# Kernel optimization log

Hardware: AMD Instinct MI355X
Metric: run time of the kernel (lower is better)

## Reference

```python
import jax, jax.numpy as jnp
import numpy as np
import math

B, S, IN_DIM = 4, 2048, 256
ATT_DIM, NUM_HEADS, TOP_K = 128, 4, 32


def _linear_params(key, out_dim, in_dim):
    kw, kb = jax.random.split(key)
    bound = 1.0 / math.sqrt(in_dim)
    w = jax.random.uniform(kw, (out_dim, in_dim), jnp.float32, -bound, bound)
    b = jax.random.uniform(kb, (out_dim,), jnp.float32, -bound, bound)
    return w, b


def setup_inputs() -> dict:
    key = jax.random.key(0)
    keys = jax.random.split(key, 16)
    x = jax.random.normal(keys[0], (B, S, IN_DIM), jnp.float32)
    tp_w, tp_b = _linear_params(keys[1], ATT_DIM, IN_DIM)
    sp_w, sp_b = _linear_params(keys[2], ATT_DIM, IN_DIM)
    ta_qw, ta_qb = _linear_params(keys[3], ATT_DIM, ATT_DIM)
    ta_kw, ta_kb = _linear_params(keys[4], ATT_DIM, ATT_DIM)
    ta_vw, ta_vb = _linear_params(keys[5], ATT_DIM, ATT_DIM)
    ta_ow, ta_ob = _linear_params(keys[6], ATT_DIM, ATT_DIM)
    sa_qw, sa_qb = _linear_params(keys[7], ATT_DIM, ATT_DIM)
    sa_kw, sa_kb = _linear_params(keys[8], ATT_DIM, ATT_DIM)
    sa_vw, sa_vb = _linear_params(keys[9], ATT_DIM, ATT_DIM)
    sa_ow, sa_ob = _linear_params(keys[10], ATT_DIM, ATT_DIM)
    gate_w, gate_b = _linear_params(keys[11], ATT_DIM, 2 * ATT_DIM)
    fus_w, fus_b = _linear_params(keys[12], ATT_DIM, 2 * ATT_DIM)
    return dict(x=x, tp_w=tp_w, tp_b=tp_b, sp_w=sp_w, sp_b=sp_b,
                ta_qw=ta_qw, ta_qb=ta_qb, ta_kw=ta_kw, ta_kb=ta_kb,
                ta_vw=ta_vw, ta_vb=ta_vb, ta_ow=ta_ow, ta_ob=ta_ob,
                sa_qw=sa_qw, sa_qb=sa_qb, sa_kw=sa_kw, sa_kb=sa_kb,
                sa_vw=sa_vw, sa_vb=sa_vb, sa_ow=sa_ow, sa_ob=sa_ob,
                gate_w=gate_w, gate_b=gate_b, fus_w=fus_w, fus_b=fus_b)


def _lin(x, w, b):
    return x @ w.T + b


def _sparse_topk_attention(x, qw, qb, kw, kb, vw, vb, ow, ob):
    # x: [B, S, E]; dropout is identity in eval mode
    b, s, e = x.shape
    h, d = NUM_HEADS, e // NUM_HEADS
    q = _lin(x, qw, qb).reshape(b, s, h, d).transpose(0, 2, 1, 3)  # [B,H,S,D]
    k = _lin(x, kw, kb).reshape(b, s, h, d).transpose(0, 2, 1, 3)
    v = _lin(x, vw, vb).reshape(b, s, h, d).transpose(0, 2, 1, 3)
    scores = jnp.einsum('bhqd,bhkd->bhqk', q, k) / math.sqrt(d)  # [B,H,S,S]
    kk = min(TOP_K, s)
    top_scores, top_idx = jax.lax.top_k(scores, kk)  # [B,H,S,K]
    soft = jax.nn.softmax(top_scores, axis=-1)
    # scatter softmaxed top-k weights into a zero [B,H,S,S] matrix (faithful to source)
    bi = jnp.arange(b)[:, None, None, None]
    hi = jnp.arange(h)[None, :, None, None]
    si = jnp.arange(s)[None, None, :, None]
    sparse = jnp.zeros_like(scores).at[bi, hi, si, top_idx].set(soft)
    out = jnp.einsum('bhqk,bhkd->bhqd', sparse, v)
    out = out.transpose(0, 2, 1, 3).reshape(b, s, e)
    return _lin(out, ow, ob)


def reference(x, tp_w, tp_b, sp_w, sp_b,
              ta_qw, ta_qb, ta_kw, ta_kb, ta_vw, ta_vb, ta_ow, ta_ob,
              sa_qw, sa_qb, sa_kw, sa_kb, sa_vw, sa_vb, sa_ow, sa_ob,
              gate_w, gate_b, fus_w, fus_b):
    temporal = _lin(x, tp_w, tp_b)
    temporal = _sparse_topk_attention(temporal, ta_qw, ta_qb, ta_kw, ta_kb,
                                      ta_vw, ta_vb, ta_ow, ta_ob)
    semantic = _lin(x, sp_w, sp_b)
    semantic = _sparse_topk_attention(semantic, sa_qw, sa_qb, sa_kw, sa_kb,
                                      sa_vw, sa_vb, sa_ow, sa_ob)
    concat = jnp.concatenate([temporal, semantic], axis=-1)  # [B,S,2A]
    gate = jax.nn.sigmoid(_lin(concat, gate_w, gate_b))
    fused = _lin(concat, fus_w, fus_b) * gate
    return fused
```

## Files before the change

### kernel.cpp

```cpp
#include <hip/hip_runtime.h>
#include <math.h>

#define B_   4
#define S_   2048
#define AD   128
#define NH   4
#define HD   32
#define TK   32
#define SEG  1048576
#define CAP  192

#define OFF_PROJ 0
#define OFF_Q    (1 * SEG)
#define OFF_K    (2 * SEG)
#define OFF_V    (3 * SEG)
#define OFF_ATT  (4 * SEG)
#define OFF_T    (5 * SEG)
#define OFF_SB   (6 * SEG)
#define OFF_CAT  (7 * SEG)

__device__ float g_ws[9 * SEG];
__device__ float g_sc[8 * S_ * S_];

__device__ __forceinline__ unsigned f2key(float s) {
    unsigned u = __float_as_uint(s);
    return (u & 0x80000000u) ? ~u : (u | 0x80000000u);
}
__device__ __forceinline__ float key2f(unsigned k) {
    unsigned u = (k & 0x80000000u) ? (k & 0x7FFFFFFFu) : ~k;
    return __uint_as_float(u);
}

template <int KD>
__global__ __launch_bounds__(256)
void lin_kernel(const float* __restrict__ Xext, int xoff,
                const float* __restrict__ W, const float* __restrict__ Bv,
                int yoff)
{
    const float* X = Xext ? Xext : (const float*)(g_ws + xoff);
    float* Y = g_ws + yoff;
    __shared__ float Xs[32][68];
    __shared__ float Ws[32][68];
    const int bm = blockIdx.x * 64;
    const int bn = blockIdx.y * 64;
    const int t  = threadIdx.x;
    const int tx = t & 15, ty = t >> 4;
    const int sr = t >> 3, sc4 = t & 7;
    float acc[4][4] = {};
    for (int kk = 0; kk < KD; kk += 32) {
        #pragma unroll
        for (int it = 0; it < 2; ++it) {
            int rr = sr + it * 32;
            float4 xa = *(const float4*)(X + (size_t)(bm + rr) * KD + kk + sc4 * 4);
            float4 wa = *(const float4*)(W + (size_t)(bn + rr) * KD + kk + sc4 * 4);
            Xs[sc4*4+0][rr] = xa.x; Xs[sc4*4+1][rr] = xa.y;
            Xs[sc4*4+2][rr] = xa.z; Xs[sc4*4+3][rr] = xa.w;
            Ws[sc4*4+0][rr] = wa.x; Ws[sc4*4+1][rr] = wa.y;
            Ws[sc4*4+2][rr] = wa.z; Ws[sc4*4+3][rr] = wa.w;
        }
        __syncthreads();
        #pragma unroll
        for (int kc = 0; kc < 32; ++kc) {
            float4 a4 = *(const float4*)&Xs[kc][ty * 4];
            float4 b4 = *(const float4*)&Ws[kc][tx * 4];
            float a[4] = {a4.x, a4.y, a4.z, a4.w};
            float bb[4] = {b4.x, b4.y, b4.z, b4.w};
            #pragma unroll
            for (int i = 0; i < 4; ++i)
                #pragma unroll
                for (int j = 0; j < 4; ++j)
                    acc[i][j] = fmaf(a[i], bb[j], acc[i][j]);
        }
        __syncthreads();
    }
    #pragma unroll
    for (int i = 0; i < 4; ++i) {
        int row = bm + ty * 4 + i;
        int col = bn + tx * 4;
        float4 o;
        o.x = acc[i][0] + Bv[col + 0]; o.y = acc[i][1] + Bv[col + 1];
        o.z = acc[i][2] + Bv[col + 2]; o.w = acc[i][3] + Bv[col + 3];
        *(float4*)(Y + (size_t)row * AD + col) = o;
    }
}

template <int KD>
__global__ __launch_bounds__(256)
void lin3_kernel(int xoff,
                 const float* __restrict__ W0, const float* __restrict__ B0, int y0,
                 const float* __restrict__ W1, const float* __restrict__ B1, int y1,
                 const float* __restrict__ W2, const float* __restrict__ B2, int y2)
{
    const int z = blockIdx.z;
    const float* X = (const float*)(g_ws + xoff);
    const float* W = (z == 0) ? W0 : (z == 1) ? W1 : W2;
    const float* Bv = (z == 0) ? B0 : (z == 1) ? B1 : B2;
    float* Y = g_ws + ((z == 0) ? y0 : (z == 1) ? y1 : y2);
    __shared__ float Xs[32][68];
    __shared__ float Ws[32][68];
    const int bm = blockIdx.x * 64;
    const int bn = blockIdx.y * 64;
    const int t  = threadIdx.x;
    const int tx = t & 15, ty = t >> 4;
    const int sr = t >> 3, sc4 = t & 7;
    float acc[4][4] = {};
    for (int kk = 0; kk < KD; kk += 32) {
        #pragma unroll
        for (int it = 0; it < 2; ++it) {
            int rr = sr + it * 32;
            float4 xa = *(const float4*)(X + (size_t)(bm + rr) * KD + kk + sc4 * 4);
            float4 wa = *(const float4*)(W + (size_t)(bn + rr) * KD + kk + sc4 * 4);
            Xs[sc4*4+0][rr] = xa.x; Xs[sc4*4+1][rr] = xa.y;
            Xs[sc4*4+2][rr] = xa.z; Xs[sc4*4+3][rr] = xa.w;
            Ws[sc4*4+0][rr] = wa.x; Ws[sc4*4+1][rr] = wa.y;
            Ws[sc4*4+2][rr] = wa.z; Ws[sc4*4+3][rr] = wa.w;
        }
        __syncthreads();
        #pragma unroll
        for (int kc = 0; kc < 32; ++kc) {
            float4 a4 = *(const float4*)&Xs[kc][ty * 4];
            float4 b4 = *(const float4*)&Ws[kc][tx * 4];
            float a[4] = {a4.x, a4.y, a4.z, a4.w};
            float bb[4] = {b4.x, b4.y, b4.z, b4.w};
            #pragma unroll
            for (int i = 0; i < 4; ++i)
                #pragma unroll
                for (int j = 0; j < 4; ++j)
                    acc[i][j] = fmaf(a[i], bb[j], acc[i][j]);
        }
        __syncthreads();
    }
    #pragma unroll
    for (int i = 0; i < 4; ++i) {
        int row = bm + ty * 4 + i;
        int col = bn + tx * 4;
        float4 o;
        o.x = acc[i][0] + Bv[col + 0]; o.y = acc[i][1] + Bv[col + 1];
        o.z = acc[i][2] + Bv[col + 2]; o.w = acc[i][3] + Bv[col + 3];
        *(float4*)(Y + (size_t)row * AD + col) = o;
    }
}

__global__ __launch_bounds__(256)
void score_kernel(int qoff, int koff, int chunk)
{
    const int zh = blockIdx.z;
    const int hh = chunk * 8 + zh, b = hh >> 2, h = hh & 3;
    const float* Qb = g_ws + qoff + (size_t)b * S_ * AD + h * HD;
    const float* Kb = g_ws + koff + (size_t)b * S_ * AD + h * HD;
    float* Sc = g_sc + (size_t)zh * S_ * S_;
    __shared__ float Qs[32][68];
    __shared__ float Ks[32][68];
    const int t = threadIdx.x, tx = t & 15, ty = t >> 4;
    const int sr = t >> 3, sc4 = t & 7;
    const int q0 = blockIdx.y * 64, k0 = blockIdx.x * 64;
    #pragma unroll
    for (int it = 0; it < 2; ++it) {
        int rr = sr + it * 32;
        float4 qa = *(const float4*)(Qb + (size_t)(q0 + rr) * AD + sc4 * 4);
        float4 ka = *(const float4*)(Kb + (size_t)(k0 + rr) * AD + sc4 * 4);
        Qs[sc4*4+0][rr] = qa.x; Qs[sc4*4+1][rr] = qa.y;
        Qs[sc4*4+2][rr] = qa.z; Qs[sc4*4+3][rr] = qa.w;
        Ks[sc4*4+0][rr] = ka.x; Ks[sc4*4+1][rr] = ka.y;
        Ks[sc4*4+2][rr] = ka.z; Ks[sc4*4+3][rr] = ka.w;
    }
    __syncthreads();
    float acc[4][4] = {};
    #pragma unroll
    for (int kc = 0; kc < 32; ++kc) {
        float4 a4 = *(const float4*)&Qs[kc][ty * 4];
        float4 b4 = *(const float4*)&Ks[kc][tx * 4];
        float a[4] = {a4.x, a4.y, a4.z, a4.w};
        float bb[4] = {b4.x, b4.y, b4.z, b4.w};
        #pragma unroll
        for (int i = 0; i < 4; ++i)
            #pragma unroll
            for (int j = 0; j < 4; ++j)
                acc[i][j] = fmaf(a[i], bb[j], acc[i][j]);
    }
    const float scale = 0.17677669529663688f;
    #pragma unroll
    for (int i = 0; i < 4; ++i) {
        float4 o;
        o.x = acc[i][0] * scale; o.y = acc[i][1] * scale;
        o.z = acc[i][2] * scale; o.w = acc[i][3] * scale;
        *(float4*)(Sc + (size_t)(q0 + ty * 4 + i) * S_ + k0 + tx * 4) = o;
    }
}

__global__ __launch_bounds__(256)
void topk_kernel(int voff, int ooff, int chunk)
{
    const float* V = g_ws + voff;
    float* O = g_ws + ooff;

    __shared__ unsigned long long sve[4][CAP];
    __shared__ float    wsel[4][32];
    __shared__ unsigned jsel[4][32];

    const int wid  = threadIdx.x >> 6;
    const int lane = threadIdx.x & 63;
    const int gr   = blockIdx.x * 4 + wid;
    const int zh   = gr >> 11, q = gr & 2047;
    const int hh   = chunk * 8 + zh;
    const int b    = hh >> 2,  h = hh & 3;

    unsigned long long* sv = sve[wid];
    float*    wp = wsel[wid];
    unsigned* jp = jsel[wid];

    const float* Srow  = g_sc + (size_t)zh * S_ * S_ + (size_t)q * S_;
    const float* vbase = V + (size_t)b * S_ * AD + h * HD;

    float4 s4[8];
    #pragma unroll
    for (int i = 0; i < 8; ++i) s4[i] = ((const float4*)Srow)[i * 64 + lane];
    unsigned keys[32];
    unsigned lmax = 0u;
    #pragma unroll
    for (int i = 0; i < 8; ++i) {
        unsigned k0 = f2key(s4[i].x), k1 = f2key(s4[i].y);
        unsigned k2 = f2key(s4[i].z), k3 = f2key(s4[i].w);
        keys[i * 4 + 0] = k0; keys[i * 4 + 1] = k1;
        keys[i * 4 + 2] = k2; keys[i * 4 + 3] = k3;
        unsigned m01 = (k0 > k1) ? k0 : k1;
        unsigned m23 = (k2 > k3) ? k2 : k3;
        unsigned m = (m01 > m23) ? m01 : m23;
        lmax = (m > lmax) ? m : lmax;
    }

    unsigned bs = lmax;
    #pragma unroll
    for (int k = 2; k <= 64; k <<= 1) {
        #pragma unroll
        for (int j = k >> 1; j > 0; j >>= 1) {
            unsigned o = (unsigned)__shfl_xor((int)bs, j);
            bool up = ((lane & k) == 0);
            bool lower = ((lane & j) == 0);
            bs = (up == lower) ? (bs < o ? bs : o) : (bs > o ? bs : o);
        }
    }
    const unsigned thr  = (unsigned)__shfl((int)bs, 32);
    const unsigned mkey = (unsigned)__shfl((int)bs, 63);
    const float Mf = key2f(mkey);

    int base = 0;
    const unsigned long long lt = (1ull << lane) - 1ull;
    #pragma unroll
    for (int t = 0; t < 32; ++t) {
        bool pred = keys[t] >= thr;
        unsigned long long m = __ballot(pred);
        int slot = base + __popcll(m & lt);
        if (pred && slot < CAP) {
            unsigned jidx = (unsigned)((t >> 2) * 256 + lane * 4 + (t & 3));
            sv[slot] = ((unsigned long long)keys[t] << 32) | (unsigned)(2047 - jidx);
        }
        base += __popcll(m);
    }
    const int S = base;
    asm volatile("s_waitcnt lgkmcnt(0)" ::: "memory");

    if (S <= 64) {
        unsigned long long pi = (lane < S) ? sv[lane] : 0ull;
        int rank = 0;
        for (int jx = 0; jx < S; ++jx)
            rank += (sv[jx] > pi) ? 1 : 0;
        float e = 0.f; unsigned ji = 0;
        if (lane < S && rank < TK) {
            float val = key2f((unsigned)(pi >> 32));
            e = __expf(val - Mf);
            ji = 2047u - (unsigned)(pi & 0xFFFFFFFFull);
        }
        float esum = e;
        #pragma unroll
        for (int off = 1; off < 64; off <<= 1) esum += __shfl_xor(esum, off);
        if (lane < S && rank < TK) { wp[rank] = e / esum; jp[rank] = ji; }
    } else if (S <= CAP) {
        unsigned long long pi[3]; int rk[3]; float ee[3]; unsigned jj[3];
        float esum = 0.f;
        #pragma unroll
        for (int u = 0; u < 3; ++u) {
            int i = lane + u * 64;
            pi[u] = (i < S) ? sv[i] : 0ull;
            rk[u] = 0; ee[u] = 0.f; jj[u] = 0;
        }
        for (int jx = 0; jx < S; ++jx) {
            unsigned long long pj = sv[jx];
            #pragma unroll
            for (int u = 0; u < 3; ++u)
                rk[u] += (pj > pi[u]) ? 1 : 0;
        }
        #pragma unroll
        for (int u = 0; u < 3; ++u) {
            int i = lane + u * 64;
            if (i < S && rk[u] < TK) {
                float val = key2f((unsigned)(pi[u] >> 32));
                ee[u] = __expf(val - Mf);
                jj[u] = 2047u - (unsigned)(pi[u] & 0xFFFFFFFFull);
                esum += ee[u];
            }
        }
        #pragma unroll
        for (int off = 1; off < 64; off <<= 1) esum += __shfl_xor(esum, off);
        #pragma unroll
        for (int u = 0; u < 3; ++u) {
            int i = lane + u * 64;
            if (i < S && rk[u] < TK) { wp[rk[u]] = ee[u] / esum; jp[rk[u]] = jj[u]; }
        }
    } else {
        unsigned consumed = 0u;
        for (int i = 0; i < TK; ++i) {
            unsigned bk = 0u; unsigned gj = 0xFFFFFFFFu;
            #pragma unroll
            for (int t = 0; t < 32; ++t) {
                if (((consumed >> t) & 1u) == 0u) {
                    unsigned kk = keys[t];
                    unsigned j = (unsigned)((t >> 2) * 256 + lane * 4 + (t & 3));
                    if (kk > bk || (kk == bk && j < gj)) { bk = kk; gj = j; }
                }
            }
            #pragma unroll
            for (int off = 1; off < 64; off <<= 1) {
                unsigned ok = (unsigned)__shfl_xor((int)bk, off);
                unsigned oj = (unsigned)__shfl_xor((int)gj, off);
                if (ok > bk || (ok == bk && oj < gj)) { bk = ok; gj = oj; }
            }
            if (((gj >> 2) & 63u) == (unsigned)lane && gj != 0xFFFFFFFFu) {
                int t = ((int)gj >> 8) * 4 + ((int)gj & 3);
                consumed |= (1u << t);
            }
            if (lane == 0) { wp[i] = key2f(bk); jp[i] = gj; }
        }
        asm volatile("s_waitcnt lgkmcnt(0)" ::: "memory");
        float v = (lane < TK) ? wp[lane] : 0.f;
        float e = (lane < TK) ? __expf(v - Mf) : 0.f;
        float esum = e;
        #pragma unroll
        for (int off = 1; off < 64; off <<= 1) esum += __shfl_xor(esum, off);
        if (lane < TK) wp[lane] = e / esum;
    }
    asm volatile("s_waitcnt lgkmcnt(0)" ::: "memory");

    float oacc = 0.f;
    const int dd = lane & 31, half = lane >> 5;
    #pragma unroll
    for (int u2 = 0; u2 < 16; ++u2) {
        int i = half * 16 + u2;
        oacc = fmaf(wp[i], vbase[(size_t)jp[i] * AD + dd], oacc);
    }
    oacc += __shfl_down(oacc, 32);
    if (lane < HD) O[((size_t)b * S_ + q) * AD + h * HD + lane] = oacc;
}

__global__ __launch_bounds__(256)
void concat_kernel()
{
    int i = blockIdx.x * 256 + threadIdx.x;
    int row = i >> 8, c = i & 255;
    float v = (c < AD) ? g_ws[OFF_T + row * AD + c]
                       : g_ws[OFF_SB + row * AD + (c - AD)];
    g_ws[OFF_CAT + i] = v;
}

__global__ __launch_bounds__(256)
void fuse_kernel(float* __restrict__ out)
{
    int i = blockIdx.x * 256 + threadIdx.x;
    float g = g_ws[OFF_Q + i];
    float f = g_ws[OFF_K + i];
    out[i] = f / (1.0f + expf(-g));
}

extern "C" void kernel_launch(void* const* d_in, const int* in_sizes, int n_in,
                              void* d_out, int out_size, void* d_ws, size_t ws_size,
                              hipStream_t stream)
{
    (void)in_sizes; (void)n_in; (void)d_ws; (void)ws_size; (void)out_size;
    const float* x      = (const float*)d_in[0];
    const float* tp_w   = (const float*)d_in[1];
    const float* tp_b   = (const float*)d_in[2];
    const float* sp_w   = (const float*)d_in[3];
    const float* sp_b   = (const float*)d_in[4];
    const float* gate_w = (const float*)d_in[21];
    const float* gate_b = (const float*)d_in[22];
    const float* fus_w  = (const float*)d_in[23];
    const float* fus_b  = (const float*)d_in[24];

    dim3 gl(128, 2);
    for (int br = 0; br < 2; ++br) {
        const float* pw = br ? sp_w : tp_w;
        const float* pb = br ? sp_b : tp_b;
        int base = 5 + br * 8;
        const float* qw = (const float*)d_in[base + 0];
        const float* qb = (const float*)d_in[base + 1];
        const float* kw = (const float*)d_in[base + 2];
        const float* kb = (const float*)d_in[base + 3];
        const float* vw = (const float*)d_in[base + 4];
        const float* vb = (const float*)d_in[base + 5];
        const float* ow = (const float*)d_in[base + 6];
        const float* ob = (const float*)d_in[base + 7];

        lin_kernel<256><<<gl, 256, 0, stream>>>(x, 0, pw, pb, OFF_PROJ);
        lin3_kernel<128><<<dim3(128, 2, 3), 256, 0, stream>>>(
            OFF_PROJ, qw, qb, OFF_Q, kw, kb, OFF_K, vw, vb, OFF_V);
        for (int chunk = 0; chunk < 2; ++chunk) {
            score_kernel<<<dim3(32, 32, 8), 256, 0, stream>>>(OFF_Q, OFF_K, chunk);
            topk_kernel<<<4096, 256, 0, stream>>>(OFF_V, OFF_ATT, chunk);
        }
        lin_kernel<128><<<gl, 256, 0, stream>>>(nullptr, OFF_ATT, ow, ob,
                                                br ? OFF_SB : OFF_T);
    }
    concat_kernel<<<8192, 256, 0, stream>>>();
    lin3_kernel<256><<<dim3(128, 2, 2), 256, 0, stream>>>(
        OFF_CAT, gate_w, gate_b, OFF_Q, fus_w, fus_b, OFF_K,
        (const float*)nullptr, (const float*)nullptr, 0);
    fuse_kernel<<<4096, 256, 0, stream>>>((float*)d_out);
}
```

Before: 373.3 us.

## Process two score rows per wavefront in top-k and pad shared tiles

The top-k kernel now handles two query rows per wavefront. Both rows' keys are loaded and their bitonic threshold searches run interleaved, then selection runs per row, and each half-wave does the V gather for one row, which removes the cross-half shuffle reduction. This is meant to add instruction-level parallelism and halve the grid. The cost is doubled register use for keys (64 per lane), which may lower occupancy. Separately, the shared-memory tile padding changes from 68 to 72 floats in the GEMM and score kernels to alter the bank-conflict pattern.

```diff
diff --git a/kernel.cpp b/kernel.cpp
--- a/kernel.cpp
+++ b/kernel.cpp
@@ -39,8 +39,8 @@
 {
     const float* X = Xext ? Xext : (const float*)(g_ws + xoff);
     float* Y = g_ws + yoff;
-    __shared__ float Xs[32][68];
-    __shared__ float Ws[32][68];
+    __shared__ float Xs[32][72];
+    __shared__ float Ws[32][72];
     const int bm = blockIdx.x * 64;
     const int bn = blockIdx.y * 64;
     const int t  = threadIdx.x;
@@ -96,8 +96,8 @@
     const float* W = (z == 0) ? W0 : (z == 1) ? W1 : W2;
     const float* Bv = (z == 0) ? B0 : (z == 1) ? B1 : B2;
     float* Y = g_ws + ((z == 0) ? y0 : (z == 1) ? y1 : y2);
-    __shared__ float Xs[32][68];
-    __shared__ float Ws[32][68];
+    __shared__ float Xs[32][72];
+    __shared__ float Ws[32][72];
     const int bm = blockIdx.x * 64;
     const int bn = blockIdx.y * 64;
     const int t  = threadIdx.x;
@@ -149,8 +149,8 @@
     const float* Qb = g_ws + qoff + (size_t)b * S_ * AD + h * HD;
     const float* Kb = g_ws + koff + (size_t)b * S_ * AD + h * HD;
     float* Sc = g_sc + (size_t)zh * S_ * S_;
-    __shared__ float Qs[32][68];
-    __shared__ float Ks[32][68];
+    __shared__ float Qs[32][72];
+    __shared__ float Ks[32][72];
     const int t = threadIdx.x, tx = t & 15, ty = t >> 4;
     const int sr = t >> 3, sc4 = t & 7;
     const int q0 = blockIdx.y * 64, k0 = blockIdx.x * 64;
@@ -188,62 +188,11 @@
     }
 }
 
-__global__ __launch_bounds__(256)
-void topk_kernel(int voff, int ooff, int chunk)
-{
-    const float* V = g_ws + voff;
-    float* O = g_ws + ooff;
-
-    __shared__ unsigned long long sve[4][CAP];
-    __shared__ float    wsel[4][32];
-    __shared__ unsigned jsel[4][32];
-
-    const int wid  = threadIdx.x >> 6;
-    const int lane = threadIdx.x & 63;
-    const int gr   = blockIdx.x * 4 + wid;
-    const int zh   = gr >> 11, q = gr & 2047;
-    const int hh   = chunk * 8 + zh;
-    const int b    = hh >> 2,  h = hh & 3;
-
-    unsigned long long* sv = sve[wid];
-    float*    wp = wsel[wid];
-    unsigned* jp = jsel[wid];
-
-    const float* Srow  = g_sc + (size_t)zh * S_ * S_ + (size_t)q * S_;
-    const float* vbase = V + (size_t)b * S_ * AD + h * HD;
-
-    float4 s4[8];
-    #pragma unroll
-    for (int i = 0; i < 8; ++i) s4[i] = ((const float4*)Srow)[i * 64 + lane];
-    unsigned keys[32];
-    unsigned lmax = 0u;
-    #pragma unroll
-    for (int i = 0; i < 8; ++i) {
-        unsigned k0 = f2key(s4[i].x), k1 = f2key(s4[i].y);
-        unsigned k2 = f2key(s4[i].z), k3 = f2key(s4[i].w);
-        keys[i * 4 + 0] = k0; keys[i * 4 + 1] = k1;
-        keys[i * 4 + 2] = k2; keys[i * 4 + 3] = k3;
-        unsigned m01 = (k0 > k1) ? k0 : k1;
-        unsigned m23 = (k2 > k3) ? k2 : k3;
-        unsigned m = (m01 > m23) ? m01 : m23;
-        lmax = (m > lmax) ? m : lmax;
-    }
-
-    unsigned bs = lmax;
-    #pragma unroll
-    for (int k = 2; k <= 64; k <<= 1) {
-        #pragma unroll
-        for (int j = k >> 1; j > 0; j >>= 1) {
-            unsigned o = (unsigned)__shfl_xor((int)bs, j);
-            bool up = ((lane & k) == 0);
-            bool lower = ((lane & j) == 0);
-            bs = (up == lower) ? (bs < o ? bs : o) : (bs > o ? bs : o);
-        }
-    }
-    const unsigned thr  = (unsigned)__shfl((int)bs, 32);
-    const unsigned mkey = (unsigned)__shfl((int)bs, 63);
-    const float Mf = key2f(mkey);
-
+__device__ __forceinline__ void select_row(const unsigned (&keys)[32],
+                                           unsigned long long* sv,
+                                           float* wp, unsigned* jp,
+                                           int lane, unsigned thr, float Mf)
+{
     int base = 0;
     const unsigned long long lt = (1ull << lane) - 1ull;
     #pragma unroll
@@ -340,16 +289,83 @@
         if (lane < TK) wp[lane] = e / esum;
     }
     asm volatile("s_waitcnt lgkmcnt(0)" ::: "memory");
-
+}
+
+__global__ __launch_bounds__(256)
+void topk_kernel(int voff, int ooff, int chunk)
+{
+    const float* V = g_ws + voff;
+    float* O = g_ws + ooff;
+
+    __shared__ unsigned long long sve[4][2][CAP];
+    __shared__ float    wsel[4][2][32];
+    __shared__ unsigned jsel[4][2][32];
+
+    const int wid  = threadIdx.x >> 6;
+    const int lane = threadIdx.x & 63;
+    const int gr   = blockIdx.x * 4 + wid;
+    const int row0 = gr * 2;
+    const int zh   = row0 >> 11;
+    const int q0   = row0 & 2047, q1 = q0 + 1;
+    const int hh   = chunk * 8 + zh;
+    const int b    = hh >> 2,  h = hh & 3;
+
+    const float* Srow0 = g_sc + (size_t)zh * S_ * S_ + (size_t)q0 * S_;
+    const float* Srow1 = Srow0 + S_;
+    const float* vbase = V + (size_t)b * S_ * AD + h * HD;
+
+    unsigned keys0[32], keys1[32];
+    unsigned lmax0 = 0u, lmax1 = 0u;
+    #pragma unroll
+    for (int i = 0; i < 8; ++i) {
+        float4 s4 = ((const float4*)Srow0)[i * 64 + lane];
+        unsigned k0 = f2key(s4.x), k1 = f2key(s4.y);
+        unsigned k2 = f2key(s4.z), k3 = f2key(s4.w);
+        keys0[i*4+0] = k0; keys0[i*4+1] = k1; keys0[i*4+2] = k2; keys0[i*4+3] = k3;
+        unsigned m01 = (k0 > k1) ? k0 : k1, m23 = (k2 > k3) ? k2 : k3;
+        unsigned m = (m01 > m23) ? m01 : m23;
+        lmax0 = (m > lmax0) ? m : lmax0;
+    }
+    #pragma unroll
+    for (int i = 0; i < 8; ++i) {
+        float4 s4 = ((const float4*)Srow1)[i * 64 + lane];
+        unsigned k0 = f2key(s4.x), k1 = f2key(s4.y);
+        unsigned k2 = f2key(s4.z), k3 = f2key(s4.w);
+        keys1[i*4+0] = k0; keys1[i*4+1] = k1; keys1[i*4+2] = k2; keys1[i*4+3] = k3;
+        unsigned m01 = (k0 > k1) ? k0 : k1, m23 = (k2 > k3) ? k2 : k3;
+        unsigned m = (m01 > m23) ? m01 : m23;
+        lmax1 = (m > lmax1) ? m : lmax1;
+    }
+
+    unsigned bs0 = lmax0, bs1 = lmax1;
+    #pragma unroll
+    for (int k = 2; k <= 64; k <<= 1) {
+        #pragma unroll
+        for (int j = k >> 1; j > 0; j >>= 1) {
+            unsigned o0 = (unsigned)__shfl_xor((int)bs0, j);
+            unsigned o1 = (unsigned)__shfl_xor((int)bs1, j);
+            bool keepmin = (((lane & k) == 0) == ((lane & j) == 0));
+            bs0 = keepmin ? (bs0 < o0 ? bs0 : o0) : (bs0 > o0 ? bs0 : o0);
+            bs1 = keepmin ? (bs1 < o1 ? bs1 : o1) : (bs1 > o1 ? bs1 : o1);
+        }
+    }
+    const unsigned thr0 = (unsigned)__shfl((int)bs0, 32);
+    const unsigned thr1 = (unsigned)__shfl((int)bs1, 32);
+    const float Mf0 = key2f((unsigned)__shfl((int)bs0, 63));
+    const float Mf1 = key2f((unsigned)__shfl((int)bs1, 63));
+
+    select_row(keys0, sve[wid][0], wsel[wid][0], jsel[wid][0], lane, thr0, Mf0);
+    select_row(keys1, sve[wid][1], wsel[wid][1], jsel[wid][1], lane, thr1, Mf1);
+
+    const int dd = lane & 31, half = lane >> 5;
+    const float*    wp = wsel[wid][half];
+    const unsigned* jp = jsel[wid][half];
     float oacc = 0.f;
-    const int dd = lane & 31, half = lane >> 5;
-    #pragma unroll
-    for (int u2 = 0; u2 < 16; ++u2) {
-        int i = half * 16 + u2;
+    #pragma unroll
+    for (int i = 0; i < 32; ++i)
         oacc = fmaf(wp[i], vbase[(size_t)jp[i] * AD + dd], oacc);
-    }
-    oacc += __shfl_down(oacc, 32);
-    if (lane < HD) O[((size_t)b * S_ + q) * AD + h * HD + lane] = oacc;
+    const int qq = half ? q1 : q0;
+    O[((size_t)b * S_ + qq) * AD + h * HD + dd] = oacc;
 }
 
 __global__ __launch_bounds__(256)
@@ -405,7 +421,7 @@
             OFF_PROJ, qw, qb, OFF_Q, kw, kb, OFF_K, vw, vb, OFF_V);
         for (int chunk = 0; chunk < 2; ++chunk) {
             score_kernel<<<dim3(32, 32, 8), 256, 0, stream>>>(OFF_Q, OFF_K, chunk);
-            topk_kernel<<<4096, 256, 0, stream>>>(OFF_V, OFF_ATT, chunk);
+            topk_kernel<<<2048, 256, 0, stream>>>(OFF_V, OFF_ATT, chunk);
         }
         lin_kernel<128><<<gl, 256, 0, stream>>>(nullptr, OFF_ATT, ow, ob,
                                                 br ? OFF_SB : OFF_T);
```

New measurement: 429.0 us. 14.9% more time.

## Swizzle shared-memory tiles and halve score-buffer chunk size

Applied to the files above, without the earlier changes.

Applies an XOR swizzle to the transposed shared-memory tiles in the linear and score GEMM kernels to reduce LDS bank conflicts. It also cuts the per-launch head chunk from 8 to 4, shrinking the global score scratch buffer so it is more likely to stay cache-resident between the score and top-k passes. The cost is twice as many score/top-k launches, with smaller grids per launch.

```diff
diff --git a/kernel.cpp b/kernel.cpp
--- a/kernel.cpp
+++ b/kernel.cpp
@@ -9,6 +9,7 @@
 #define TK   32
 #define SEG  1048576
 #define CAP  192
+#define CHD  4
 
 #define OFF_PROJ 0
 #define OFF_Q    (1 * SEG)
@@ -20,7 +21,7 @@
 #define OFF_CAT  (7 * SEG)
 
 __device__ float g_ws[9 * SEG];
-__device__ float g_sc[8 * S_ * S_];
+__device__ float g_sc[CHD * S_ * S_];
 
 __device__ __forceinline__ unsigned f2key(float s) {
     unsigned u = __float_as_uint(s);
@@ -46,23 +47,26 @@
     const int t  = threadIdx.x;
     const int tx = t & 15, ty = t >> 4;
     const int sr = t >> 3, sc4 = t & 7;
+    const int ssw = sc4 << 2;
     float acc[4][4] = {};
     for (int kk = 0; kk < KD; kk += 32) {
         #pragma unroll
         for (int it = 0; it < 2; ++it) {
             int rr = sr + it * 32;
+            int rs = rr ^ ssw;
             float4 xa = *(const float4*)(X + (size_t)(bm + rr) * KD + kk + sc4 * 4);
             float4 wa = *(const float4*)(W + (size_t)(bn + rr) * KD + kk + sc4 * 4);
-            Xs[sc4*4+0][rr] = xa.x; Xs[sc4*4+1][rr] = xa.y;
-            Xs[sc4*4+2][rr] = xa.z; Xs[sc4*4+3][rr] = xa.w;
-            Ws[sc4*4+0][rr] = wa.x; Ws[sc4*4+1][rr] = wa.y;
-            Ws[sc4*4+2][rr] = wa.z; Ws[sc4*4+3][rr] = wa.w;
+            Xs[sc4*4+0][rs] = xa.x; Xs[sc4*4+1][rs] = xa.y;
+            Xs[sc4*4+2][rs] = xa.z; Xs[sc4*4+3][rs] = xa.w;
+            Ws[sc4*4+0][rs] = wa.x; Ws[sc4*4+1][rs] = wa.y;
+            Ws[sc4*4+2][rs] = wa.z; Ws[sc4*4+3][rs] = wa.w;
         }
         __syncthreads();
         #pragma unroll
         for (int kc = 0; kc < 32; ++kc) {
-            float4 a4 = *(const float4*)&Xs[kc][ty * 4];
-            float4 b4 = *(const float4*)&Ws[kc][tx * 4];
+            const int swz = ((kc >> 2) & 7) << 2;
+            float4 a4 = *(const float4*)&Xs[kc][(ty * 4) ^ swz];
+            float4 b4 = *(const float4*)&Ws[kc][(tx * 4) ^ swz];
             float a[4] = {a4.x, a4.y, a4.z, a4.w};
             float bb[4] = {b4.x, b4.y, b4.z, b4.w};
             #pragma unroll
@@ -103,23 +107,26 @@
     const int t  = threadIdx.x;
     const int tx = t & 15, ty = t >> 4;
     const int sr = t >> 3, sc4 = t & 7;
+    const int ssw = sc4 << 2;
     float acc[4][4] = {};
     for (int kk = 0; kk < KD; kk += 32) {
         #pragma unroll
         for (int it = 0; it < 2; ++it) {
             int rr = sr + it * 32;
+            int rs = rr ^ ssw;
             float4 xa = *(const float4*)(X + (size_t)(bm + rr) * KD + kk + sc4 * 4);
             float4 wa = *(const float4*)(W + (size_t)(bn + rr) * KD + kk + sc4 * 4);
-            Xs[sc4*4+0][rr] = xa.x; Xs[sc4*4+1][rr] = xa.y;
-            Xs[sc4*4+2][rr] = xa.z; Xs[sc4*4+3][rr] = xa.w;
-            Ws[sc4*4+0][rr] = wa.x; Ws[sc4*4+1][rr] = wa.y;
-            Ws[sc4*4+2][rr] = wa.z; Ws[sc4*4+3][rr] = wa.w;
+            Xs[sc4*4+0][rs] = xa.x; Xs[sc4*4+1][rs] = xa.y;
+            Xs[sc4*4+2][rs] = xa.z; Xs[sc4*4+3][rs] = xa.w;
+            Ws[sc4*4+0][rs] = wa.x; Ws[sc4*4+1][rs] = wa.y;
+            Ws[sc4*4+2][rs] = wa.z; Ws[sc4*4+3][rs] = wa.w;
         }
         __syncthreads();
         #pragma unroll
         for (int kc = 0; kc < 32; ++kc) {
-            float4 a4 = *(const float4*)&Xs[kc][ty * 4];
-            float4 b4 = *(const float4*)&Ws[kc][tx * 4];
+            const int swz = ((kc >> 2) & 7) << 2;
+            float4 a4 = *(const float4*)&Xs[kc][(ty * 4) ^ swz];
+            float4 b4 = *(const float4*)&Ws[kc][(tx * 4) ^ swz];
             float a[4] = {a4.x, a4.y, a4.z, a4.w};
             float bb[4] = {b4.x, b4.y, b4.z, b4.w};
             #pragma unroll
@@ -145,7 +152,7 @@
 void score_kernel(int qoff, int koff, int chunk)
 {
     const int zh = blockIdx.z;
-    const int hh = chunk * 8 + zh, b = hh >> 2, h = hh & 3;
+    const int hh = chunk * CHD + zh, b = hh >> 2, h = hh & 3;
     const float* Qb = g_ws + qoff + (size_t)b * S_ * AD + h * HD;
     const float* Kb = g_ws + koff + (size_t)b * S_ * AD + h * HD;
     float* Sc = g_sc + (size_t)zh * S_ * S_;
@@ -153,23 +160,26 @@
     __shared__ float Ks[32][68];
     const int t = threadIdx.x, tx = t & 15, ty = t >> 4;
     const int sr = t >> 3, sc4 = t & 7;
+    const int ssw = sc4 << 2;
     const int q0 = blockIdx.y * 64, k0 = blockIdx.x * 64;
     #pragma unroll
     for (int it = 0; it < 2; ++it) {
         int rr = sr + it * 32;
+        int rs = rr ^ ssw;
         float4 qa = *(const float4*)(Qb + (size_t)(q0 + rr) * AD + sc4 * 4);
         float4 ka = *(const float4*)(Kb + (size_t)(k0 + rr) * AD + sc4 * 4);
-        Qs[sc4*4+0][rr] = qa.x; Qs[sc4*4+1][rr] = qa.y;
-        Qs[sc4*4+2][rr] = qa.z; Qs[sc4*4+3][rr] = qa.w;
-        Ks[sc4*4+0][rr] = ka.x; Ks[sc4*4+1][rr] = ka.y;
-        Ks[sc4*4+2][rr] = ka.z; Ks[sc4*4+3][rr] = ka.w;
+        Qs[sc4*4+0][rs] = qa.x; Qs[sc4*4+1][rs] = qa.y;
+        Qs[sc4*4+2][rs] = qa.z; Qs[sc4*4+3][rs] = qa.w;
+        Ks[sc4*4+0][rs] = ka.x; Ks[sc4*4+1][rs] = ka.y;
+        Ks[sc4*4+2][rs] = ka.z; Ks[sc4*4+3][rs] = ka.w;
     }
     __syncthreads();
     float acc[4][4] = {};
     #pragma unroll
     for (int kc = 0; kc < 32; ++kc) {
-        float4 a4 = *(const float4*)&Qs[kc][ty * 4];
-        float4 b4 = *(const float4*)&Ks[kc][tx * 4];
+        const int swz = ((kc >> 2) & 7) << 2;
+        float4 a4 = *(const float4*)&Qs[kc][(ty * 4) ^ swz];
+        float4 b4 = *(const float4*)&Ks[kc][(tx * 4) ^ swz];
         float a[4] = {a4.x, a4.y, a4.z, a4.w};
         float bb[4] = {b4.x, b4.y, b4.z, b4.w};
         #pragma unroll
@@ -202,7 +212,7 @@
     const int lane = threadIdx.x & 63;
     const int gr   = blockIdx.x * 4 + wid;
     const int zh   = gr >> 11, q = gr & 2047;
-    const int hh   = chunk * 8 + zh;
+    const int hh   = chunk * CHD + zh;
     const int b    = hh >> 2,  h = hh & 3;
 
     unsigned long long* sv = sve[wid];
@@ -403,9 +413,9 @@
         lin_kernel<256><<<gl, 256, 0, stream>>>(x, 0, pw, pb, OFF_PROJ);
         lin3_kernel<128><<<dim3(128, 2, 3), 256, 0, stream>>>(
             OFF_PROJ, qw, qb, OFF_Q, kw, kb, OFF_K, vw, vb, OFF_V);
-        for (int chunk = 0; chunk < 2; ++chunk) {
-            score_kernel<<<dim3(32, 32, 8), 256, 0, stream>>>(OFF_Q, OFF_K, chunk);
-            topk_kernel<<<4096, 256, 0, stream>>>(OFF_V, OFF_ATT, chunk);
+        for (int chunk = 0; chunk < 4; ++chunk) {
+            score_kernel<<<dim3(32, 32, CHD), 256, 0, stream>>>(OFF_Q, OFF_K, chunk);
+            topk_kernel<<<CHD * 512, 256, 0, stream>>>(OFF_V, OFF_ATT, chunk);
         }
         lin_kernel<128><<<gl, 256, 0, stream>>>(nullptr, OFF_ATT, ow, ob,
                                                 br ? OFF_SB : OFF_T);
```

Result: slower. 442.8 us (+18.6%).

## Software-pipeline score and top-k stages in one interleaved kernel

Applied to the files above, without the earlier changes.

Merges the score GEMM and top-k/softmax/gather kernels into one pipe_kernel whose blocks are split between computing scores for the next chunk and running top-k on the previous chunk. Double-buffered score storage lets the two stages run concurrently, so compute-bound score tiles overlap with memory- and latency-bound top-k work. Both branches' Q/K/V projections are computed up front into separate buffers so chunks from the two attention branches can be chained. The cost is more workspace memory, shared memory sized to the larger role, and some divergence in the per-block role choice.

```diff
diff --git a/kernel.cpp b/kernel.cpp
--- a/kernel.cpp
+++ b/kernel.cpp
@@ -11,16 +11,20 @@
 #define CAP  192
 
 #define OFF_PROJ 0
-#define OFF_Q    (1 * SEG)
-#define OFF_K    (2 * SEG)
-#define OFF_V    (3 * SEG)
-#define OFF_ATT  (4 * SEG)
-#define OFF_T    (5 * SEG)
-#define OFF_SB   (6 * SEG)
-#define OFF_CAT  (7 * SEG)
-
-__device__ float g_ws[9 * SEG];
-__device__ float g_sc[8 * S_ * S_];
+#define OFF_QT  (1 * SEG)
+#define OFF_KT  (2 * SEG)
+#define OFF_VT  (3 * SEG)
+#define OFF_QS  (4 * SEG)
+#define OFF_KS  (5 * SEG)
+#define OFF_VS  (6 * SEG)
+#define OFF_AT  (7 * SEG)
+#define OFF_AS  (8 * SEG)
+#define OFF_T   (9 * SEG)
+#define OFF_SB  (10 * SEG)
+#define OFF_CAT (11 * SEG)
+
+__device__ float g_ws[13 * SEG];
+__device__ float g_sc[2][8 * S_ * S_];
 
 __device__ __forceinline__ unsigned f2key(float s) {
     unsigned u = __float_as_uint(s);
@@ -142,214 +146,223 @@
 }
 
 __global__ __launch_bounds__(256)
-void score_kernel(int qoff, int koff, int chunk)
-{
-    const int zh = blockIdx.z;
-    const int hh = chunk * 8 + zh, b = hh >> 2, h = hh & 3;
-    const float* Qb = g_ws + qoff + (size_t)b * S_ * AD + h * HD;
-    const float* Kb = g_ws + koff + (size_t)b * S_ * AD + h * HD;
-    float* Sc = g_sc + (size_t)zh * S_ * S_;
-    __shared__ float Qs[32][68];
-    __shared__ float Ks[32][68];
-    const int t = threadIdx.x, tx = t & 15, ty = t >> 4;
-    const int sr = t >> 3, sc4 = t & 7;
-    const int q0 = blockIdx.y * 64, k0 = blockIdx.x * 64;
-    #pragma unroll
-    for (int it = 0; it < 2; ++it) {
-        int rr = sr + it * 32;
-        float4 qa = *(const float4*)(Qb + (size_t)(q0 + rr) * AD + sc4 * 4);
-        float4 ka = *(const float4*)(Kb + (size_t)(k0 + rr) * AD + sc4 * 4);
-        Qs[sc4*4+0][rr] = qa.x; Qs[sc4*4+1][rr] = qa.y;
-        Qs[sc4*4+2][rr] = qa.z; Qs[sc4*4+3][rr] = qa.w;
-        Ks[sc4*4+0][rr] = ka.x; Ks[sc4*4+1][rr] = ka.y;
-        Ks[sc4*4+2][rr] = ka.z; Ks[sc4*4+3][rr] = ka.w;
+void pipe_kernel(int nscore, int ntopk,
+                 int s_qoff, int s_koff, int s_chunk, int s_buf,
+                 int t_voff, int t_ooff, int t_chunk, int t_buf)
+{
+    __shared__ __align__(16) unsigned char smem[17408];
+    const int bid = blockIdx.x;
+    bool isScore;
+    int rid;
+    if (nscore > 0 && ntopk > 0) {
+        if ((bid % 3) == 2) { isScore = false; rid = bid / 3; }
+        else                { isScore = true;  rid = (bid / 3) * 2 + (bid % 3); }
+    } else if (nscore > 0) { isScore = true;  rid = bid; }
+    else                   { isScore = false; rid = bid; }
+
+    if (isScore) {
+        float (*Qs)[68] = (float(*)[68])smem;
+        float (*Ks)[68] = (float(*)[68])(smem + 8704);
+        const int kx = rid & 31, qy = (rid >> 5) & 31, zh = rid >> 10;
+        const int hh = s_chunk * 8 + zh, b = hh >> 2, h = hh & 3;
+        const float* Qb = g_ws + s_qoff + (size_t)b * S_ * AD + h * HD;
+        const float* Kb = g_ws + s_koff + (size_t)b * S_ * AD + h * HD;
+        float* Sc = g_sc[s_buf] + (size_t)zh * S_ * S_;
+        const int t = threadIdx.x, tx = t & 15, ty = t >> 4;
+        const int sr = t >> 3, sc4 = t & 7;
+        const int q0 = qy * 64, k0 = kx * 64;
+        #pragma unroll
+        for (int it = 0; it < 2; ++it) {
+            int rr = sr + it * 32;
+            float4 qa = *(const float4*)(Qb + (size_t)(q0 + rr) * AD + sc4 * 4);
+            float4 ka = *(const float4*)(Kb + (size_t)(k0 + rr) * AD + sc4 * 4);
+            Qs[sc4*4+0][rr] = qa.x; Qs[sc4*4+1][rr] = qa.y;
+            Qs[sc4*4+2][rr] = qa.z; Qs[sc4*4+3][rr] = qa.w;
+            Ks[sc4*4+0][rr] = ka.x; Ks[sc4*4+1][rr] = ka.y;
+            Ks[sc4*4+2][rr] = ka.z; Ks[sc4*4+3][rr] = ka.w;
+        }
+        __syncthreads();
+        float acc[4][4] = {};
+        #pragma unroll
+        for (int kc = 0; kc < 32; ++kc) {
+            float4 a4 = *(const float4*)&Qs[kc][ty * 4];
+            float4 b4 = *(const float4*)&Ks[kc][tx * 4];
+            float a[4] = {a4.x, a4.y, a4.z, a4.w};
+            float bb[4] = {b4.x, b4.y, b4.z, b4.w};
+            #pragma unroll
+            for (int i = 0; i < 4; ++i)
+                #pragma unroll
+                for (int j = 0; j < 4; ++j)
+                    acc[i][j] = fmaf(a[i], bb[j], acc[i][j]);
+        }
+        const float scale = 0.17677669529663688f;
+        #pragma unroll
+        for (int i = 0; i < 4; ++i) {
+            float4 o;
+            o.x = acc[i][0] * scale; o.y = acc[i][1] * scale;
+            o.z = acc[i][2] * scale; o.w = acc[i][3] * scale;
+            *(float4*)(Sc + (size_t)(q0 + ty * 4 + i) * S_ + k0 + tx * 4) = o;
+        }
+    } else {
+        unsigned long long* sve = (unsigned long long*)smem;
+        float*    wsel = (float*)(smem + 6144);
+        unsigned* jsel = (unsigned*)(smem + 6656);
+        const float* V = g_ws + t_voff;
+        float* O = g_ws + t_ooff;
+
+        const int wid  = threadIdx.x >> 6;
+        const int lane = threadIdx.x & 63;
+        const int gr   = rid * 4 + wid;
+        const int zh   = gr >> 11, q = gr & 2047;
+        const int hh   = t_chunk * 8 + zh;
+        const int b    = hh >> 2,  h = hh & 3;
+
+        unsigned long long* sv = sve + wid * CAP;
+        float*    wp = wsel + wid * 32;
+        unsigned* jp = jsel + wid * 32;
+
+        const float* Srow  = g_sc[t_buf] + (size_t)zh * S_ * S_ + (size_t)q * S_;
+        const float* vbase = V + (size_t)b * S_ * AD + h * HD;
+
+        float4 s4[8];
+        #pragma unroll
+        for (int i = 0; i < 8; ++i) s4[i] = ((const float4*)Srow)[i * 64 + lane];
+        unsigned keys[32];
+        unsigned lmax = 0u;
+        #pragma unroll
+        for (int i = 0; i < 8; ++i) {
+            unsigned k0 = f2key(s4[i].x), k1 = f2key(s4[i].y);
+            unsigned k2 = f2key(s4[i].z), k3 = f2key(s4[i].w);
+            keys[i * 4 + 0] = k0; keys[i * 4 + 1] = k1;
+            keys[i * 4 + 2] = k2; keys[i * 4 + 3] = k3;
+            unsigned m01 = (k0 > k1) ? k0 : k1;
+            unsigned m23 = (k2 > k3) ? k2 : k3;
+            unsigned m = (m01 > m23) ? m01 : m23;
+            lmax = (m > lmax) ? m : lmax;
+        }
+
+        unsigned bs = lmax;
+        #pragma unroll
+        for (int k = 2; k <= 64; k <<= 1) {
+            #pragma unroll
+            for (int j = k >> 1; j > 0; j >>= 1) {
+                unsigned o = (unsigned)__shfl_xor((int)bs, j);
+                bool up = ((lane & k) == 0);
+                bool lower = ((lane & j) == 0);
+                bs = (up == lower) ? (bs < o ? bs : o) : (bs > o ? bs : o);
+            }
+        }
+        const unsigned thr  = (unsigned)__shfl((int)bs, 32);
+        const unsigned mkey = (unsigned)__shfl((int)bs, 63);
+        const float Mf = key2f(mkey);
+
+        int base = 0;
+        const unsigned long long lt = (1ull << lane) - 1ull;
+        #pragma unroll
+        for (int t = 0; t < 32; ++t) {
+            bool pred = keys[t] >= thr;
+            unsigned long long m = __ballot(pred);
+            int slot = base + __popcll(m & lt);
+            if (pred && slot < CAP) {
+                unsigned jidx = (unsigned)((t >> 2) * 256 + lane * 4 + (t & 3));
+                sv[slot] = ((unsigned long long)keys[t] << 32) | (unsigned)(2047 - jidx);
+            }
+            base += __popcll(m);
+        }
+        const int S = base;
+        asm volatile("s_waitcnt lgkmcnt(0)" ::: "memory");
+
+        if (S <= 64) {
+            unsigned long long pi = (lane < S) ? sv[lane] : 0ull;
+            int rank = 0;
+            for (int jx = 0; jx < S; ++jx)
+                rank += (sv[jx] > pi) ? 1 : 0;
+            float e = 0.f; unsigned ji = 0;
+            if (lane < S && rank < TK) {
+                float val = key2f((unsigned)(pi >> 32));
+                e = __expf(val - Mf);
+                ji = 2047u - (unsigned)(pi & 0xFFFFFFFFull);
+            }
+            float esum = e;
+            #pragma unroll
+            for (int off = 1; off < 64; off <<= 1) esum += __shfl_xor(esum, off);
+            if (lane < S && rank < TK) { wp[rank] = e / esum; jp[rank] = ji; }
+        } else if (S <= CAP) {
+            unsigned long long pi[3]; int rk[3]; float ee[3]; unsigned jj[3];
+            float esum = 0.f;
+            #pragma unroll
+            for (int u = 0; u < 3; ++u) {
+                int i = lane + u * 64;
+                pi[u] = (i < S) ? sv[i] : 0ull;
+                rk[u] = 0; ee[u] = 0.f; jj[u] = 0;
+            }
+            for (int jx = 0; jx < S; ++jx) {
+                unsigned long long pj = sv[jx];
+                #pragma unroll
+                for (int u = 0; u < 3; ++u)
+                    rk[u] += (pj > pi[u]) ? 1 : 0;
+            }
+            #pragma unroll
+            for (int u = 0; u < 3; ++u) {
+                int i = lane + u * 64;
+                if (i < S && rk[u] < TK) {
+                    float val = key2f((unsigned)(pi[u] >> 32));
+                    ee[u] = __expf(val - Mf);
+                    jj[u] = 2047u - (unsigned)(pi[u] & 0xFFFFFFFFull);
+                    esum += ee[u];
+                }
+            }
+            #pragma unroll
+            for (int off = 1; off < 64; off <<= 1) esum += __shfl_xor(esum, off);
+            #pragma unroll
+            for (int u = 0; u < 3; ++u) {
+                int i = lane + u * 64;
+                if (i < S && rk[u] < TK) { wp[rk[u]] = ee[u] / esum; jp[rk[u]] = jj[u]; }
+            }
+        } else {
+            unsigned consumed = 0u;
+            for (int i = 0; i < TK; ++i) {
+                unsigned bk = 0u; unsigned gj = 0xFFFFFFFFu;
+                #pragma unroll
+                for (int t = 0; t < 32; ++t) {
+                    if (((consumed >> t) & 1u) == 0u) {
+                        unsigned kk = keys[t];
+                        unsigned j = (unsigned)((t >> 2) * 256 + lane * 4 + (t & 3));
+                        if (kk > bk || (kk == bk && j < gj)) { bk = kk; gj = j; }
+                    }
+                }
+                #pragma unroll
+                for (int off = 1; off < 64; off <<= 1) {
+                    unsigned ok = (unsigned)__shfl_xor((int)bk, off);
+                    unsigned oj = (unsigned)__shfl_xor((int)gj, off);
+                    if (ok > bk || (ok == bk && oj < gj)) { bk = ok; gj = oj; }
+                }
+                if (((gj >> 2) & 63u) == (unsigned)lane && gj != 0xFFFFFFFFu) {
+                    int t = ((int)gj >> 8) * 4 + ((int)gj & 3);
+                    consumed |= (1u << t);
+                }
+                if (lane == 0) { wp[i] = key2f(bk); jp[i] = gj; }
+            }
+            asm volatile("s_waitcnt lgkmcnt(0)" ::: "memory");
+            float v = (lane < TK) ? wp[lane] : 0.f;
+            float e = (lane < TK) ? __expf(v - Mf) : 0.f;
+            float esum = e;
+            #pragma unroll
+            for (int off = 1; off < 64; off <<= 1) esum += __shfl_xor(esum, off);
+            if (lane < TK) wp[lane] = e / esum;
+        }
+        asm volatile("s_waitcnt lgkmcnt(0)" ::: "memory");
+
+        float oacc = 0.f;
+        const int dd = lane & 31, half = lane >> 5;
+        #pragma unroll
+        for (int u2 = 0; u2 < 16; ++u2) {
+            int i = half * 16 + u2;
+            oacc = fmaf(wp[i], vbase[(size_t)jp[i] * AD + dd], oacc);
+        }
+        oacc += __shfl_down(oacc, 32);
+        if (lane < HD) O[((size_t)b * S_ + q) * AD + h * HD + lane] = oacc;
     }
-    __syncthreads();
-    float acc[4][4] = {};
-    #pragma unroll
-    for (int kc = 0; kc < 32; ++kc) {
-        float4 a4 = *(const float4*)&Qs[kc][ty * 4];
-        float4 b4 = *(const float4*)&Ks[kc][tx * 4];
-        float a[4] = {a4.x, a4.y, a4.z, a4.w};
-        float bb[4] = {b4.x, b4.y, b4.z, b4.w};
-        #pragma unroll
-        for (int i = 0; i < 4; ++i)
-            #pragma unroll
-            for (int j = 0; j < 4; ++j)
-                acc[i][j] = fmaf(a[i], bb[j], acc[i][j]);
-    }
-    const float scale = 0.17677669529663688f;
-    #pragma unroll
-    for (int i = 0; i < 4; ++i) {
-        float4 o;
-        o.x = acc[i][0] * scale; o.y = acc[i][1] * scale;
-        o.z = acc[i][2] * scale; o.w = acc[i][3] * scale;
-        *(float4*)(Sc + (size_t)(q0 + ty * 4 + i) * S_ + k0 + tx * 4) = o;
-    }
-}
-
-__global__ __launch_bounds__(256)
-void topk_kernel(int voff, int ooff, int chunk)
-{
-    const float* V = g_ws + voff;
-    float* O = g_ws + ooff;
-
-    __shared__ unsigned long long sve[4][CAP];
-    __shared__ float    wsel[4][32];
-    __shared__ unsigned jsel[4][32];
-
-    const int wid  = threadIdx.x >> 6;
-    const int lane = threadIdx.x & 63;
-    const int gr   = blockIdx.x * 4 + wid;
-    const int zh   = gr >> 11, q = gr & 2047;
-    const int hh   = chunk * 8 + zh;
-    const int b    = hh >> 2,  h = hh & 3;
-
-    unsigned long long* sv = sve[wid];
-    float*    wp = wsel[wid];
-    unsigned* jp = jsel[wid];
-
-    const float* Srow  = g_sc + (size_t)zh * S_ * S_ + (size_t)q * S_;
-    const float* vbase = V + (size_t)b * S_ * AD + h * HD;
-
-    float4 s4[8];
-    #pragma unroll
-    for (int i = 0; i < 8; ++i) s4[i] = ((const float4*)Srow)[i * 64 + lane];
-    unsigned keys[32];
-    unsigned lmax = 0u;
-    #pragma unroll
-    for (int i = 0; i < 8; ++i) {
-        unsigned k0 = f2key(s4[i].x), k1 = f2key(s4[i].y);
-        unsigned k2 = f2key(s4[i].z), k3 = f2key(s4[i].w);
-        keys[i * 4 + 0] = k0; keys[i * 4 + 1] = k1;
-        keys[i * 4 + 2] = k2; keys[i * 4 + 3] = k3;
-        unsigned m01 = (k0 > k1) ? k0 : k1;
-        unsigned m23 = (k2 > k3) ? k2 : k3;
-        unsigned m = (m01 > m23) ? m01 : m23;
-        lmax = (m > lmax) ? m : lmax;
-    }
-
-    unsigned bs = lmax;
-    #pragma unroll
-    for (int k = 2; k <= 64; k <<= 1) {
-        #pragma unroll
-        for (int j = k >> 1; j > 0; j >>= 1) {
-            unsigned o = (unsigned)__shfl_xor((int)bs, j);
-            bool up = ((lane & k) == 0);
-            bool lower = ((lane & j) == 0);
-            bs = (up == lower) ? (bs < o ? bs : o) : (bs > o ? bs : o);
-        }
-    }
-    const unsigned thr  = (unsigned)__shfl((int)bs, 32);
-    const unsigned mkey = (unsigned)__shfl((int)bs, 63);
-    const float Mf = key2f(mkey);
-
-    int base = 0;
-    const unsigned long long lt = (1ull << lane) - 1ull;
-    #pragma unroll
-    for (int t = 0; t < 32; ++t) {
-        bool pred = keys[t] >= thr;
-        unsigned long long m = __ballot(pred);
-        int slot = base + __popcll(m & lt);
-        if (pred && slot < CAP) {
-            unsigned jidx = (unsigned)((t >> 2) * 256 + lane * 4 + (t & 3));
-            sv[slot] = ((unsigned long long)keys[t] << 32) | (unsigned)(2047 - jidx);
-        }
-        base += __popcll(m);
-    }
-    const int S = base;
-    asm volatile("s_waitcnt lgkmcnt(0)" ::: "memory");
-
-    if (S <= 64) {
-        unsigned long long pi = (lane < S) ? sv[lane] : 0ull;
-        int rank = 0;
-        for (int jx = 0; jx < S; ++jx)
-            rank += (sv[jx] > pi) ? 1 : 0;
-        float e = 0.f; unsigned ji = 0;
-        if (lane < S && rank < TK) {
-            float val = key2f((unsigned)(pi >> 32));
-            e = __expf(val - Mf);
-            ji = 2047u - (unsigned)(pi & 0xFFFFFFFFull);
-        }
-        float esum = e;
-        #pragma unroll
-        for (int off = 1; off < 64; off <<= 1) esum += __shfl_xor(esum, off);
-        if (lane < S && rank < TK) { wp[rank] = e / esum; jp[rank] = ji; }
-    } else if (S <= CAP) {
-        unsigned long long pi[3]; int rk[3]; float ee[3]; unsigned jj[3];
-        float esum = 0.f;
-        #pragma unroll
-        for (int u = 0; u < 3; ++u) {
-            int i = lane + u * 64;
-            pi[u] = (i < S) ? sv[i] : 0ull;
-            rk[u] = 0; ee[u] = 0.f; jj[u] = 0;
-        }
-        for (int jx = 0; jx < S; ++jx) {
-            unsigned long long pj = sv[jx];
-            #pragma unroll
-            for (int u = 0; u < 3; ++u)
-                rk[u] += (pj > pi[u]) ? 1 : 0;
-        }
-        #pragma unroll
-        for (int u = 0; u < 3; ++u) {
-            int i = lane + u * 64;
-            if (i < S && rk[u] < TK) {
-                float val = key2f((unsigned)(pi[u] >> 32));
-                ee[u] = __expf(val - Mf);
-                jj[u] = 2047u - (unsigned)(pi[u] & 0xFFFFFFFFull);
-                esum += ee[u];
-            }
-        }
-        #pragma unroll
-        for (int off = 1; off < 64; off <<= 1) esum += __shfl_xor(esum, off);
-        #pragma unroll
-        for (int u = 0; u < 3; ++u) {
-            int i = lane + u * 64;
-            if (i < S && rk[u] < TK) { wp[rk[u]] = ee[u] / esum; jp[rk[u]] = jj[u]; }
-        }
-    } else {
-        unsigned consumed = 0u;
-        for (int i = 0; i < TK; ++i) {
-            unsigned bk = 0u; unsigned gj = 0xFFFFFFFFu;
-            #pragma unroll
-            for (int t = 0; t < 32; ++t) {
-                if (((consumed >> t) & 1u) == 0u) {
-                    unsigned kk = keys[t];
-                    unsigned j = (unsigned)((t >> 2) * 256 + lane * 4 + (t & 3));
-                    if (kk > bk || (kk == bk && j < gj)) { bk = kk; gj = j; }
-                }
-            }
-            #pragma unroll
-            for (int off = 1; off < 64; off <<= 1) {
-                unsigned ok = (unsigned)__shfl_xor((int)bk, off);
-                unsigned oj = (unsigned)__shfl_xor((int)gj, off);
-                if (ok > bk || (ok == bk && oj < gj)) { bk = ok; gj = oj; }
-            }
-            if (((gj >> 2) & 63u) == (unsigned)lane && gj != 0xFFFFFFFFu) {
-                int t = ((int)gj >> 8) * 4 + ((int)gj & 3);
-                consumed |= (1u << t);
-            }
-            if (lane == 0) { wp[i] = key2f(bk); jp[i] = gj; }
-        }
-        asm volatile("s_waitcnt lgkmcnt(0)" ::: "memory");
-        float v = (lane < TK) ? wp[lane] : 0.f;
-        float e = (lane < TK) ? __expf(v - Mf) : 0.f;
-        float esum = e;
-        #pragma unroll
-        for (int off = 1; off < 64; off <<= 1) esum += __shfl_xor(esum, off);
-        if (lane < TK) wp[lane] = e / esum;
-    }
-    asm volatile("s_waitcnt lgkmcnt(0)" ::: "memory");
-
-    float oacc = 0.f;
-    const int dd = lane & 31, half = lane >> 5;
-    #pragma unroll
-    for (int u2 = 0; u2 < 16; ++u2) {
-        int i = half * 16 + u2;
-        oacc = fmaf(wp[i], vbase[(size_t)jp[i] * AD + dd], oacc);
-    }
-    oacc += __shfl_down(oacc, 32);
-    if (lane < HD) O[((size_t)b * S_ + q) * AD + h * HD + lane] = oacc;
 }
 
 __global__ __launch_bounds__(256)
@@ -366,8 +379,8 @@
 void fuse_kernel(float* __restrict__ out)
 {
     int i = blockIdx.x * 256 + threadIdx.x;
-    float g = g_ws[OFF_Q + i];
-    float f = g_ws[OFF_K + i];
+    float g = g_ws[OFF_QT + i];
+    float f = g_ws[OFF_KT + i];
     out[i] = f / (1.0f + expf(-g));
 }
 
@@ -386,33 +399,37 @@
     const float* fus_w  = (const float*)d_in[23];
     const float* fus_b  = (const float*)d_in[24];
 
+    const float* ta_w[8]; const float* sa_w[8];
+    for (int i = 0; i < 8; ++i) { ta_w[i] = (const float*)d_in[5 + i];
+                                  sa_w[i] = (const float*)d_in[13 + i]; }
+
     dim3 gl(128, 2);
-    for (int br = 0; br < 2; ++br) {
-        const float* pw = br ? sp_w : tp_w;
-        const float* pb = br ? sp_b : tp_b;
-        int base = 5 + br * 8;
-        const float* qw = (const float*)d_in[base + 0];
-        const float* qb = (const float*)d_in[base + 1];
-        const float* kw = (const float*)d_in[base + 2];
-        const float* kb = (const float*)d_in[base + 3];
-        const float* vw = (const float*)d_in[base + 4];
-        const float* vb = (const float*)d_in[base + 5];
-        const float* ow = (const float*)d_in[base + 6];
-        const float* ob = (const float*)d_in[base + 7];
-
-        lin_kernel<256><<<gl, 256, 0, stream>>>(x, 0, pw, pb, OFF_PROJ);
-        lin3_kernel<128><<<dim3(128, 2, 3), 256, 0, stream>>>(
-            OFF_PROJ, qw, qb, OFF_Q, kw, kb, OFF_K, vw, vb, OFF_V);
-        for (int chunk = 0; chunk < 2; ++chunk) {
-            score_kernel<<<dim3(32, 32, 8), 256, 0, stream>>>(OFF_Q, OFF_K, chunk);
-            topk_kernel<<<4096, 256, 0, stream>>>(OFF_V, OFF_ATT, chunk);
-        }
-        lin_kernel<128><<<gl, 256, 0, stream>>>(nullptr, OFF_ATT, ow, ob,
-                                                br ? OFF_SB : OFF_T);
-    }
+    lin_kernel<256><<<gl, 256, 0, stream>>>(x, 0, tp_w, tp_b, OFF_PROJ);
+    lin3_kernel<128><<<dim3(128, 2, 3), 256, 0, stream>>>(
+        OFF_PROJ, ta_w[0], ta_w[1], OFF_QT, ta_w[2], ta_w[3], OFF_KT,
+        ta_w[4], ta_w[5], OFF_VT);
+    lin_kernel<256><<<gl, 256, 0, stream>>>(x, 0, sp_w, sp_b, OFF_PROJ);
+    lin3_kernel<128><<<dim3(128, 2, 3), 256, 0, stream>>>(
+        OFF_PROJ, sa_w[0], sa_w[1], OFF_QS, sa_w[2], sa_w[3], OFF_KS,
+        sa_w[4], sa_w[5], OFF_VS);
+
+    pipe_kernel<<<8192, 256, 0, stream>>>(8192, 0,
+        OFF_QT, OFF_KT, 0, 0,   0, 0, 0, 0);
+    pipe_kernel<<<12288, 256, 0, stream>>>(8192, 4096,
+        OFF_QT, OFF_KT, 1, 1,   OFF_VT, OFF_AT, 0, 0);
+    pipe_kernel<<<12288, 256, 0, stream>>>(8192, 4096,
+        OFF_QS, OFF_KS, 0, 0,   OFF_VT, OFF_AT, 1, 1);
+    pipe_kernel<<<12288, 256, 0, stream>>>(8192, 4096,
+        OFF_QS, OFF_KS, 1, 1,   OFF_VS, OFF_AS, 0, 0);
+    pipe_kernel<<<4096, 256, 0, stream>>>(0, 4096,
+        0, 0, 0, 0,             OFF_VS, OFF_AS, 1, 1);
+
+    lin_kernel<128><<<gl, 256, 0, stream>>>(nullptr, OFF_AT, ta_w[6], ta_w[7], OFF_T);
+    lin_kernel<128><<<gl, 256, 0, stream>>>(nullptr, OFF_AS, sa_w[6], sa_w[7], OFF_SB);
+
     concat_kernel<<<8192, 256, 0, stream>>>();
     lin3_kernel<256><<<dim3(128, 2, 2), 256, 0, stream>>>(
-        OFF_CAT, gate_w, gate_b, OFF_Q, fus_w, fus_b, OFF_K,
+        OFF_CAT, gate_w, gate_b, OFF_QT, fus_w, fus_b, OFF_KT,
         (const float*)nullptr, (const float*)nullptr, 0);
     fuse_kernel<<<4096, 256, 0, stream>>>((float*)d_out);
 }
```

Result: slower. 403.7 us (+8.1%).
